# Optimization experiments

Hardware: AMD Instinct MI355X
Metric: run time of the kernel (lower is better)

## Reference

```python
import jax, jax.numpy as jnp
import numpy as np
from itertools import product as _prod

B = 2          # batch size
NPB = 4096     # voxels per batch
C = 384        # input_dim
H = 8          # num_heads
OUT = 32       # output_dim (seg classes)
SPATIAL = (32, 256, 256)
POOL_R = np.array([1, 2, 2, 2])    # [1]+query_gs_ratio
COMP_R = np.array([1, 16, 16, 16])  # [1]+compress_ratio


def _coords():
    rng = np.random.default_rng(0)
    rows = []
    for b in range(B):
        cand = np.stack([rng.integers(0, s, 4 * NPB) for s in SPATIAL], 1)
        cand = np.unique(cand, axis=0)
        sel = cand[rng.permutation(len(cand))[:NPB]]
        rows.append(np.concatenate([np.full((NPB, 1), b, np.int64), sel], 1))
    return np.concatenate(rows).astype(np.int32)


def setup_inputs() -> dict:
    idx = _coords()                     # [N,4] unique (b,z,y,x)
    N = idx.shape[0]
    pool_u, pool_inv = np.unique(idx // POOL_R, axis=0, return_inverse=True)
    emb_u, emb_inv = np.unique(idx // COMP_R, axis=0, return_inverse=True)
    # submanifold 3x3x3 neighbor table (same batch), -1 = missing
    lut = {tuple(r): i for i, r in enumerate(idx.tolist())}
    nbr = np.full((N, 27), -1, np.int32)
    rows = idx.tolist()
    for k, (dz, dy, dx) in enumerate(_prod((-1, 0, 1), repeat=3)):
        for i, (b, z, y, x) in enumerate(rows):
            nbr[i, k] = lut.get((b, z + dz, y + dy, x + dx), -1)
    key = jax.random.key(0)
    ks = jax.random.split(key, 12)
    g = lambda k, shp, s: jax.random.normal(k, shp, jnp.float32) * s
    s = 1.0 / float(np.sqrt(C))
    return dict(
        feats=g(ks[0], (N, C), 1.0),
        W_pool=g(ks[1], (C, C), s), b_pool=jnp.zeros((C,), jnp.float32),
        W_emb=g(ks[2], (C, C), s), b_emb=jnp.zeros((C,), jnp.float32),
        Wq=g(ks[3], (C, C), s), bq=jnp.zeros((C,), jnp.float32),
        Wk=g(ks[4], (C, C), s), bk=jnp.zeros((C,), jnp.float32),
        Wv=g(ks[5], (C, C), s), bv=jnp.zeros((C,), jnp.float32),
        Wo=g(ks[6], (C, C), s), bo=jnp.zeros((C,), jnp.float32),
        W_conv=g(ks[7], (27, C, OUT), 1.0 / float(np.sqrt(27 * C))),
        b_conv=jnp.zeros((OUT,), jnp.float32),
        pool_inv=jnp.asarray(pool_inv, jnp.int32),
        pool_coords=jnp.asarray(pool_u, jnp.int32),
        emb_inv=jnp.asarray(emb_inv, jnp.int32),
        emb_coords=jnp.asarray(emb_u, jnp.int32),
        nbr_idx=jnp.asarray(nbr),
        batch_size=B,
    )


def _sine_pe(xyz, d_pos):
    # xyz: [n,3] normalized to [0,1]; PositionEmbeddingCoordsSine (3detr-style)
    cdim = d_pos // xyz.shape[1]
    dim_t = 10000.0 ** (2.0 * (jnp.arange(cdim) // 2).astype(jnp.float32) / cdim)
    emb = (xyz * (2.0 * jnp.pi))[:, :, None] / dim_t          # [n,3,cdim]
    pe = jnp.stack([jnp.sin(emb[..., 0::2]), jnp.cos(emb[..., 1::2])], -1)
    return pe.reshape(xyz.shape[0], -1)                        # [n,d_pos]


def reference(feats, W_pool, b_pool, W_emb, b_emb, Wq, bq, Wk, bk, Wv, bv,
              Wo, bo, W_conv, b_conv, pool_inv, pool_coords, emb_inv,
              emb_coords, nbr_idx, batch_size):
    Mp, Me, Cc = pool_coords.shape[0], emb_coords.shape[0], feats.shape[1]
    hd = Cc // H
    # query path: linear + scatter_max over pool cells
    pool_f = jax.ops.segment_max(feats @ W_pool + b_pool, pool_inv, num_segments=Mp)
    # kv path: linear + scatter_max over compressed cells (coords of argmax rows
    # within a cell all equal the unique cell coord, so mean == unique coord)
    emb_f = jax.ops.segment_max(feats @ W_emb + b_emb, emb_inv, num_segments=Me)
    # per-batch min/max-normalized sine positional encoding on concat(emb,pool)
    emb_xyz = emb_coords[:, 1:].astype(jnp.float32)
    pool_xyz = pool_coords[:, 1:].astype(jnp.float32)
    all_xyz = jnp.concatenate([emb_xyz, pool_xyz], 0)
    bids = jnp.concatenate([emb_coords[:, 0], pool_coords[:, 0]], 0)
    mins = jax.ops.segment_min(all_xyz, bids, num_segments=batch_size)
    maxs = jax.ops.segment_max(all_xyz, bids, num_segments=batch_size)
    norm = (all_xyz - mins[bids]) / (maxs[bids] - mins[bids] + 1e-6)
    pe = _sine_pe(norm, Cc)
    emb_f = emb_f + pe[:Me]
    pool_f = pool_f + pe[Me:]
    # multi-head cross-attention, masked to same-batch pairs
    q = (pool_f @ Wq + bq).reshape(Mp, H, hd)
    k = (emb_f @ Wk + bk).reshape(Me, H, hd)
    v = (emb_f @ Wv + bv).reshape(Me, H, hd)
    scores = jnp.einsum('phd,ehd->hpe', q, k) / jnp.sqrt(jnp.float32(hd))
    same_b = pool_coords[:, 0][None, :, None] == emb_coords[:, 0][None, None, :]
    attn = jax.nn.softmax(jnp.where(same_b, scores, -1e9), axis=-1)
    o = jnp.einsum('hpe,ehd->phd', attn, v).reshape(Mp, Cc) @ Wo + bo
    # broadcast back to voxels + residual
    new_f = feats + o[pool_inv]
    # SubMConv3d seg head: gather 27 neighbors, contract with kernel
    valid = (nbr_idx >= 0)[:, :, None]
    gathered = jnp.where(valid, new_f[jnp.maximum(nbr_idx, 0)], 0.0)  # [N,27,C]
    logits = jnp.einsum('nkc,kco->no', gathered, W_conv) + b_conv
    return logits
```

## Files before the change

kernel.cpp:

```cpp
#include <hip/hip_runtime.h>
#include <hip/hip_bf16.h>
#include <math.h>

#define CDIM 384
#define NHEAD 8
#define HD 48
#define OUTD 32
#define MAXB 16
#define CONVK 10368

typedef __bf16 bf16x8 __attribute__((ext_vector_type(8)));
typedef float f32x4 __attribute__((ext_vector_type(4)));

__device__ __forceinline__ f32x4 mfma16(bf16x8 a, bf16x8 b, f32x4 c) {
  return __builtin_amdgcn_mfma_f32_16x16x32_bf16(a, b, c, 0, 0, 0);
}
__device__ __forceinline__ bf16x8 zero8() {
  bf16x8 z = {(__bf16)0.f, (__bf16)0.f, (__bf16)0.f, (__bf16)0.f,
              (__bf16)0.f, (__bf16)0.f, (__bf16)0.f, (__bf16)0.f};
  return z;
}

__device__ __forceinline__ unsigned enc_f(float f) {
  unsigned u = __float_as_uint(f);
  return (u & 0x80000000u) ? ~u : (u | 0x80000000u);
}
__device__ __forceinline__ float dec_f(unsigned u) {
  unsigned v = (u & 0x80000000u) ? (u ^ 0x80000000u) : ~u;
  return __uint_as_float(v);
}

__global__ __launch_bounds__(256) void prep_kernel(
    const float* __restrict__ feats, __hip_bfloat16* __restrict__ feats16, int N,
    const float* __restrict__ W_pool, const float* __restrict__ W_emb,
    const float* __restrict__ Wk, const float* __restrict__ Wv,
    const float* __restrict__ Wq, const float* __restrict__ Wo,
    __hip_bfloat16* __restrict__ Wt_pe, __hip_bfloat16* __restrict__ Wt_kv,
    __hip_bfloat16* __restrict__ Wt_q, __hip_bfloat16* __restrict__ Wt_o,
    const float* __restrict__ Wc, __hip_bfloat16* __restrict__ Wct,
    __hip_bfloat16* __restrict__ vt, int Mepad,
    const int* __restrict__ ec, const int* __restrict__ pc, int Mp, int Me,
    const int* __restrict__ bsz, int* smin, int* smax, int* ebv,
    int nbF, int nbW, int nbC, int nbV, int nbM) {
  __shared__ int lmin[MAXB * 3], lmax[MAXB * 3];
  int b = blockIdx.x;
  int t = threadIdx.x;
  if (b < nbF) {
    int v = b * 256 + t;
    if (v < N * 48) {
      float4 a0 = *reinterpret_cast<const float4*>(feats + (size_t)v * 8);
      float4 a1 = *reinterpret_cast<const float4*>(feats + (size_t)v * 8 + 4);
      __hip_bfloat16 tmp[8] = {
        __float2bfloat16(a0.x), __float2bfloat16(a0.y), __float2bfloat16(a0.z), __float2bfloat16(a0.w),
        __float2bfloat16(a1.x), __float2bfloat16(a1.y), __float2bfloat16(a1.z), __float2bfloat16(a1.w)};
      *reinterpret_cast<bf16x8*>(feats16 + (size_t)v * 8) = *reinterpret_cast<const bf16x8*>(tmp);
    }
    return;
  }
  b -= nbF;
  if (b < 6 * nbW) {
    int m = b / nbW;
    int v = (b - m * nbW) * 256 + t;
    if (v >= CDIM * 48) return;
    const float* src;
    __hip_bfloat16* dst;
    switch (m) {
      case 0: src = W_pool; dst = Wt_pe; break;
      case 1: src = W_emb;  dst = Wt_pe + (size_t)CDIM * CDIM; break;
      case 2: src = Wk;     dst = Wt_kv; break;
      case 3: src = Wv;     dst = Wt_kv + (size_t)CDIM * CDIM; break;
      case 4: src = Wq;     dst = Wt_q; break;
      default: src = Wo;    dst = Wt_o; break;
    }
    int k8i = v / CDIM;
    int n = v - k8i * CDIM;
    int k8 = k8i * 8;
    __hip_bfloat16 tmp[8];
    #pragma unroll
    for (int u = 0; u < 8; ++u) tmp[u] = __float2bfloat16(src[(size_t)(k8 + u) * CDIM + n]);
    *reinterpret_cast<bf16x8*>(dst + (size_t)n * CDIM + k8) = *reinterpret_cast<const bf16x8*>(tmp);
    return;
  }
  b -= 6 * nbW;
  if (b < nbC) {
    int v = b * 256 + t;
    if (v >= OUTD * (CONVK / 8)) return;
    int k8i = v >> 5;
    int n = v & 31;
    int k8 = k8i * 8;
    __hip_bfloat16 tmp[8];
    #pragma unroll
    for (int u = 0; u < 8; ++u) tmp[u] = __float2bfloat16(Wc[(size_t)(k8 + u) * OUTD + n]);
    *reinterpret_cast<bf16x8*>(Wct + (size_t)n * CONVK + k8) = *reinterpret_cast<const bf16x8*>(tmp);
    return;
  }
  b -= nbC;
  if (b < nbV) {
    int v = b * 256 + t;
    if (v < NHEAD * Mepad) {
      int h = v / Mepad, e = v - h * Mepad;
      vt[(size_t)(h * 64 + HD) * Mepad + e] = __float2bfloat16(1.0f);
    }
    return;
  }
  b -= nbV;
  if (b < nbM) {
    if (t < MAXB * 3) { lmin[t] = 0x7fffffff; lmax[t] = (int)0x80000000; }
    __syncthreads();
    int i = b * 256 + t;
    int tot = Me + Mp;
    if (i < tot) {
      const int* r = (i < Me) ? (ec + 4 * i) : (pc + 4 * (i - Me));
      int bb = r[0];
      #pragma unroll
      for (int d = 0; d < 3; ++d) {
        atomicMin(&lmin[bb * 3 + d], r[1 + d]);
        atomicMax(&lmax[bb * 3 + d], r[1 + d]);
      }
    }
    __syncthreads();
    if (t < MAXB * 3) {
      if (lmin[t] != 0x7fffffff) atomicMin(&smin[t], lmin[t]);
      if (lmax[t] != (int)0x80000000) atomicMax(&smax[t], lmax[t]);
    }
    return;
  }
  b -= nbM;
  {
    int e = b * 256 + t;
    if (e == 0) { ebv[0] = 0; ebv[bsz[0]] = Me; }
    if (e > 0 && e < Me) {
      int b0 = ec[4 * (e - 1)], b1 = ec[4 * e];
      for (int bb = b0 + 1; bb <= b1; ++bb) ebv[bb] = e;
    }
  }
}

__global__ void pe_kernel(const unsigned* __restrict__ encP, const unsigned* __restrict__ encE,
                          __hip_bfloat16* __restrict__ pool16, __hip_bfloat16* __restrict__ emb16,
                          const int* __restrict__ pc, int Mp,
                          const int* __restrict__ ec, int Me,
                          const int* __restrict__ smin, const int* __restrict__ smax) {
  int gid = blockIdx.x * blockDim.x + threadIdx.x;
  int total = (Mp + Me) * CDIM;
  if (gid >= total) return;
  int row = gid / CDIM, c = gid - row * CDIM;
  const int* coords;
  const unsigned* src;
  __hip_bfloat16* dst;
  int lrow;
  if (row < Me) { lrow = row; coords = ec + 4 * row; src = encE; dst = emb16; }
  else { lrow = row - Me; coords = pc + 4 * lrow; src = encP; dst = pool16; }
  int b = coords[0];
  int dim = c >> 7;
  int i = c & 127;
  int j = i >> 1;
  float x = (float)coords[1 + dim];
  float mn = (float)smin[b * 3 + dim];
  float mx = (float)smax[b * 3 + dim];
  float nrm = (x - mn) / (mx - mn + 1e-6f);
  float freq = exp2f(-(float)j * 0.20762050593046014f);
  float arg = nrm * 6.283185307179586f * freq;
  float pe = (i & 1) ? cosf(arg) : sinf(arg);
  float val = dec_f(src[(size_t)lrow * CDIM + c]) + pe;
  dst[(size_t)lrow * CDIM + c] = __float2bfloat16(val);
}

template <int EPI>
__global__ __launch_bounds__(256) void mgemm_kernel(
    const __hip_bfloat16* __restrict__ A, int M,
    const __hip_bfloat16* __restrict__ Wt,
    const float* __restrict__ bias0, const float* __restrict__ bias1,
    void* __restrict__ d0, void* __restrict__ d1,
    const int* __restrict__ inv0, const int* __restrict__ inv1,
    int Mepad) {
  __shared__ __align__(16) __hip_bfloat16 As[128][72];
  __shared__ __align__(16) __hip_bfloat16 Bs[64][72];
  const int m0 = blockIdx.x * 128;
  const int n0 = blockIdx.y * 64;
  const int t = threadIdx.x;
  const int lane = t & 63, w = t >> 6;
  const int wr = w >> 1, wc = w & 1;
  const int lq = lane & 15, lg = lane >> 4;

  f32x4 acc[4][2];
  #pragma unroll
  for (int i = 0; i < 4; ++i) {
    acc[i][0] = (f32x4){0.f, 0.f, 0.f, 0.f};
    acc[i][1] = (f32x4){0.f, 0.f, 0.f, 0.f};
  }
  const int arow = t >> 3;
  const int acol = (t & 7) * 8;

  for (int k0 = 0; k0 < CDIM; k0 += 64) {
    #pragma unroll
    for (int i = 0; i < 4; ++i) {
      int r = arow + i * 32;
      int gr = m0 + r;
      bf16x8 val = zero8();
      if (gr < M) val = *reinterpret_cast<const bf16x8*>(A + (size_t)gr * CDIM + k0 + acol);
      *reinterpret_cast<bf16x8*>(&As[r][acol]) = val;
    }
    #pragma unroll
    for (int i = 0; i < 2; ++i) {
      int r = arow + i * 32;
      bf16x8 val = *reinterpret_cast<const bf16x8*>(Wt + (size_t)(n0 + r) * CDIM + k0 + acol);
      *reinterpret_cast<bf16x8*>(&Bs[r][acol]) = val;
    }
    __syncthreads();
    #pragma unroll
    for (int ks = 0; ks < 2; ++ks) {
      bf16x8 af[4], bfv[2];
      #pragma unroll
      for (int fm = 0; fm < 4; ++fm)
        af[fm] = *reinterpret_cast<const bf16x8*>(&As[wr * 64 + fm * 16 + lq][ks * 32 + lg * 8]);
      #pragma unroll
      for (int fn = 0; fn < 2; ++fn)
        bfv[fn] = *reinterpret_cast<const bf16x8*>(&Bs[wc * 32 + fn * 16 + lq][ks * 32 + lg * 8]);
      #pragma unroll
      for (int fm = 0; fm < 4; ++fm)
        #pragma unroll
        for (int fn = 0; fn < 2; ++fn)
          acc[fm][fn] = mfma16(af[fm], bfv[fn], acc[fm][fn]);
    }
    __syncthreads();
  }

  const bool sec = (n0 >= CDIM);
  const int nb = n0 - (sec ? CDIM : 0) + wc * 32;
  const int nA = nb + lq, nB = nb + 16 + lq;

  if (EPI == 0) {
    const float* bias = sec ? bias1 : bias0;
    unsigned* dst = (unsigned*)(sec ? d1 : d0);
    const int* inv = sec ? inv1 : inv0;
    float bA = bias[nA], bB = bias[nB];
    #pragma unroll
    for (int fm = 0; fm < 4; ++fm) {
      int rbase = m0 + wr * 64 + fm * 16 + lg * 4;
      int cs = -1;
      float mA = 0.f, mB = 0.f;
      #pragma unroll
      for (int j = 0; j < 4; ++j) {
        int r = rbase + j;
        if (r < M) {
          int s = inv[r];
          float vA = acc[fm][0][j] + bA;
          float vB = acc[fm][1][j] + bB;
          if (s == cs) { mA = fmaxf(mA, vA); mB = fmaxf(mB, vB); }
          else {
            if (cs >= 0) {
              atomicMax(&dst[(size_t)cs * CDIM + nA], enc_f(mA));
              atomicMax(&dst[(size_t)cs * CDIM + nB], enc_f(mB));
            }
            cs = s; mA = vA; mB = vB;
          }
        }
      }
      if (cs >= 0) {
        atomicMax(&dst[(size_t)cs * CDIM + nA], enc_f(mA));
        atomicMax(&dst[(size_t)cs * CDIM + nB], enc_f(mB));
      }
    }
  } else if (EPI == 1) {
    float bA = bias0[nA], bB = bias0[nB];
    float* dst = (float*)d0;
    #pragma unroll
    for (int fm = 0; fm < 4; ++fm)
      #pragma unroll
      for (int j = 0; j < 4; ++j) {
        int r = m0 + wr * 64 + fm * 16 + lg * 4 + j;
        if (r < M) {
          dst[(size_t)r * CDIM + nA] = acc[fm][0][j] + bA;
          dst[(size_t)r * CDIM + nB] = acc[fm][1][j] + bB;
        }
      }
  } else if (EPI == 2) {
    const float scale = 0.2082350914f;
    float bA = bias0[nA], bB = bias0[nB];
    int hA = nA / HD, dA = nA - hA * HD;
    int hB = nB / HD, dB = nB - hB * HD;
    __hip_bfloat16* dst = (__hip_bfloat16*)d0;
    #pragma unroll
    for (int fm = 0; fm < 4; ++fm)
      #pragma unroll
      for (int j = 0; j < 4; ++j) {
        int r = m0 + wr * 64 + fm * 16 + lg * 4 + j;
        if (r < M) {
          dst[(size_t)r * 512 + hA * 64 + dA] = __float2bfloat16((acc[fm][0][j] + bA) * scale);
          dst[(size_t)r * 512 + hB * 64 + dB] = __float2bfloat16((acc[fm][1][j] + bB) * scale);
        }
      }
  } else {
    if (!sec) {
      float bA = bias0[nA], bB = bias0[nB];
      int hA = nA / HD, dA = nA - hA * HD;
      int hB = nB / HD, dB = nB - hB * HD;
      __hip_bfloat16* dst = (__hip_bfloat16*)d0;
      #pragma unroll
      for (int fm = 0; fm < 4; ++fm)
        #pragma unroll
        for (int j = 0; j < 4; ++j) {
          int r = m0 + wr * 64 + fm * 16 + lg * 4 + j;
          if (r < M) {
            dst[(size_t)r * 512 + hA * 64 + dA] = __float2bfloat16(acc[fm][0][j] + bA);
            dst[(size_t)r * 512 + hB * 64 + dB] = __float2bfloat16(acc[fm][1][j] + bB);
          }
        }
    } else {
      float bA = bias1[nA], bB = bias1[nB];
      int hA = nA / HD, dA = nA - hA * HD;
      int hB = nB / HD, dB = nB - hB * HD;
      __hip_bfloat16* dst = (__hip_bfloat16*)d1;
      #pragma unroll
      for (int fm = 0; fm < 4; ++fm)
        #pragma unroll
        for (int j = 0; j < 4; ++j) {
          int r = m0 + wr * 64 + fm * 16 + lg * 4 + j;
          if (r < M) {
            dst[(size_t)(hA * 64 + dA) * Mepad + r] = __float2bfloat16(acc[fm][0][j] + bA);
            dst[(size_t)(hB * 64 + dB) * Mepad + r] = __float2bfloat16(acc[fm][1][j] + bB);
          }
        }
    }
  }
}

__global__ __launch_bounds__(256) void attn_mfma_kernel(
    const __hip_bfloat16* __restrict__ qb, const __hip_bfloat16* __restrict__ kb,
    const __hip_bfloat16* __restrict__ vt, int Mepad,
    const int* __restrict__ pc, const int* __restrict__ eb,
    int Mp, int Me, __hip_bfloat16* __restrict__ ob) {
  __shared__ __align__(16) __hip_bfloat16 Ks[64][72];
  __shared__ __align__(16) __hip_bfloat16 Vs[64][72];
  __shared__ __align__(16) __hip_bfloat16 pl[4][16][72];
  __shared__ int sred[4][4];
  const int h = blockIdx.y;
  const int t = threadIdx.x;
  const int wv = t >> 6, lane = t & 63;
  const int lq = lane & 15, lg = lane >> 4;
  const int q0 = blockIdx.x * 64 + wv * 16;

  int lo[4], hi[4];
  #pragma unroll
  for (int r = 0; r < 4; ++r) {
    int q = q0 + lg * 4 + r;
    if (q < Mp) { int b = pc[4 * q]; lo[r] = eb[b]; hi[r] = eb[b + 1]; }
    else { lo[r] = 0x7fffffff; hi[r] = 0; }
  }
  int lomin = min(min(lo[0], lo[1]), min(lo[2], lo[3]));
  int lomax = max(max(lo[0], lo[1]), max(lo[2], lo[3]));
  int himin = min(min(hi[0], hi[1]), min(hi[2], hi[3]));
  int himax = max(max(hi[0], hi[1]), max(hi[2], hi[3]));
  #pragma unroll
  for (int off = 1; off < 64; off <<= 1) {
    lomin = min(lomin, __shfl_xor(lomin, off));
    lomax = max(lomax, __shfl_xor(lomax, off));
    himin = min(himin, __shfl_xor(himin, off));
    himax = max(himax, __shfl_xor(himax, off));
  }
  if (lane == 0) {
    sred[wv][0] = lomin; sred[wv][1] = lomax;
    sred[wv][2] = himin; sred[wv][3] = himax;
  }
  __syncthreads();
  lomin = min(min(sred[0][0], sred[1][0]), min(sred[2][0], sred[3][0]));
  lomax = max(max(sred[0][1], sred[1][1]), max(sred[2][1], sred[3][1]));
  himin = min(min(sred[0][2], sred[1][2]), min(sred[2][2], sred[3][2]));
  himax = max(max(sred[0][3], sred[1][3]), max(sred[2][3], sred[3][3]));

  int qrow = min(q0 + lq, Mp - 1);
  const __hip_bfloat16* qp = qb + (size_t)qrow * 512 + h * 64 + lg * 8;
  bf16x8 aq0 = *reinterpret_cast<const bf16x8*>(qp);
  bf16x8 aq1 = *reinterpret_cast<const bf16x8*>(qp + 32);

  const int str = t >> 2;
  const int stc = (t & 3) * 16;
  const __hip_bfloat16* vrow = vt + (size_t)(h * 64 + str) * Mepad + stc;

  f32x4 zero = {0.f, 0.f, 0.f, 0.f};
  f32x4 oacc[4];
  oacc[0] = zero; oacc[1] = zero; oacc[2] = zero; oacc[3] = zero;

  bf16x8 k0, k1, v0, v1;
  auto load_tile = [&](int e0) {
    int er = e0 + str;
    k0 = zero8(); k1 = zero8();
    if (er < Me) {
      const __hip_bfloat16* kp = kb + (size_t)er * 512 + h * 64 + stc;
      k0 = *reinterpret_cast<const bf16x8*>(kp);
      k1 = *reinterpret_cast<const bf16x8*>(kp + 8);
    }
    v0 = *reinterpret_cast<const bf16x8*>(vrow + e0);
    v1 = *reinterpret_cast<const bf16x8*>(vrow + e0 + 8);
  };
  const int e0beg = lomin & ~63;
  load_tile(e0beg);

  for (int e0 = e0beg; e0 < himax; e0 += 64) {
    __syncthreads();
    *reinterpret_cast<bf16x8*>(&Ks[str][stc]) = k0;
    *reinterpret_cast<bf16x8*>(&Ks[str][stc + 8]) = k1;
    *reinterpret_cast<bf16x8*>(&Vs[str][stc]) = v0;
    *reinterpret_cast<bf16x8*>(&Vs[str][stc + 8]) = v1;
    __syncthreads();
    if (e0 + 64 < himax) load_tile(e0 + 64);

    f32x4 sf[4];
    #pragma unroll
    for (int s = 0; s < 4; ++s) {
      bf16x8 bk0 = *reinterpret_cast<const bf16x8*>(&Ks[s * 16 + lq][lg * 8]);
      bf16x8 bk1 = *reinterpret_cast<const bf16x8*>(&Ks[s * 16 + lq][32 + lg * 8]);
      f32x4 z = zero;
      z = mfma16(aq0, bk0, z);
      z = mfma16(aq1, bk1, z);
      sf[s] = z;
    }
    const bool interior = (e0 >= lomax) && (e0 + 64 <= himin);
    if (interior) {
      #pragma unroll
      for (int s = 0; s < 4; ++s)
        #pragma unroll
        for (int r = 0; r < 4; ++r)
          pl[wv][lg * 4 + r][s * 16 + lq] = __float2bfloat16(exp2f(sf[s][r]));
    } else {
      #pragma unroll
      for (int s = 0; s < 4; ++s) {
        int e = e0 + s * 16 + lq;
        #pragma unroll
        for (int r = 0; r < 4; ++r) {
          bool m = (e >= lo[r]) && (e < hi[r]);
          float p = m ? exp2f(sf[s][r]) : 0.f;
          pl[wv][lg * 4 + r][s * 16 + lq] = __float2bfloat16(p);
        }
      }
    }
    asm volatile("s_waitcnt lgkmcnt(0)" ::: "memory");
    __builtin_amdgcn_sched_barrier(0);
    #pragma unroll
    for (int ks = 0; ks < 2; ++ks) {
      bf16x8 ap = *reinterpret_cast<const bf16x8*>(&pl[wv][lq][ks * 32 + lg * 8]);
      #pragma unroll
      for (int dt = 0; dt < 4; ++dt) {
        bf16x8 bv = *reinterpret_cast<const bf16x8*>(&Vs[dt * 16 + lq][ks * 32 + lg * 8]);
        oacc[dt] = mfma16(ap, bv, oacc[dt]);
      }
    }
  }

  #pragma unroll
  for (int r = 0; r < 4; ++r) {
    float l = __shfl(oacc[3][r], (lane & 48));
    int q = q0 + lg * 4 + r;
    if (q < Mp && l > 0.f) {
      float inv = 1.0f / l;
      __hip_bfloat16* op = ob + (size_t)q * CDIM + h * HD;
      op[lq]      = __float2bfloat16(oacc[0][r] * inv);
      op[16 + lq] = __float2bfloat16(oacc[1][r] * inv);
      op[32 + lq] = __float2bfloat16(oacc[2][r] * inv);
    }
  }
}

__global__ void newf16_kernel(const float* __restrict__ feats, const float* __restrict__ o2,
                              const int* __restrict__ pinv, __hip_bfloat16* __restrict__ nf,
                              int N) {
  int v = blockIdx.x * 256 + threadIdx.x;
  if (v >= N * 48) return;
  int n = v / 48, c8 = (v - n * 48) * 8;
  const float* fp = feats + (size_t)n * CDIM + c8;
  const float* op = o2 + (size_t)pinv[n] * CDIM + c8;
  float4 a0 = *reinterpret_cast<const float4*>(fp);
  float4 a1 = *reinterpret_cast<const float4*>(fp + 4);
  float4 b0 = *reinterpret_cast<const float4*>(op);
  float4 b1 = *reinterpret_cast<const float4*>(op + 4);
  __hip_bfloat16 tmp[8] = {
    __float2bfloat16(a0.x + b0.x), __float2bfloat16(a0.y + b0.y),
    __float2bfloat16(a0.z + b0.z), __float2bfloat16(a0.w + b0.w),
    __float2bfloat16(a1.x + b1.x), __float2bfloat16(a1.y + b1.y),
    __float2bfloat16(a1.z + b1.z), __float2bfloat16(a1.w + b1.w)};
  *reinterpret_cast<bf16x8*>(nf + (size_t)v * 8) = *reinterpret_cast<const bf16x8*>(tmp);
}

__global__ __launch_bounds__(256) void mconv_kernel(
    const __hip_bfloat16* __restrict__ nf, const int* __restrict__ nbr,
    const __hip_bfloat16* __restrict__ Wct, float* __restrict__ outp, int N) {
  __shared__ __align__(16) __hip_bfloat16 As[128][72];
  __shared__ __align__(16) __hip_bfloat16 Bs[32][72];
  __shared__ int jrow[128];
  const int n0 = blockIdx.x * 128;
  const int kg = blockIdx.y;
  const int t = threadIdx.x;
  const int lane = t & 63, w = t >> 6;
  const int lq = lane & 15, lg = lane >> 4;
  f32x4 acc[2][2];
  acc[0][0] = (f32x4){0.f,0.f,0.f,0.f}; acc[0][1] = acc[0][0];
  acc[1][0] = acc[0][0]; acc[1][1] = acc[0][0];
  const int arow = t >> 3, acol = (t & 7) * 8;

  for (int kk = kg * 3; kk < kg * 3 + 3; ++kk) {
    __syncthreads();
    if (t < 128) {
      int n = n0 + t;
      jrow[t] = (n < N) ? nbr[(size_t)n * 27 + kk] : -1;
    }
    __syncthreads();
    for (int c0 = 0; c0 < CDIM; c0 += 64) {
      #pragma unroll
      for (int i = 0; i < 4; ++i) {
        int r = arow + i * 32;
        int j = jrow[r];
        bf16x8 val = zero8();
        if (j >= 0) val = *reinterpret_cast<const bf16x8*>(nf + (size_t)j * CDIM + c0 + acol);
        *reinterpret_cast<bf16x8*>(&As[r][acol]) = val;
      }
      {
        int r = t >> 3;
        bf16x8 val = *reinterpret_cast<const bf16x8*>(Wct + (size_t)r * CONVK + kk * CDIM + c0 + acol);
        *reinterpret_cast<bf16x8*>(&Bs[r][acol]) = val;
      }
      __syncthreads();
      #pragma unroll
      for (int ks = 0; ks < 2; ++ks) {
        bf16x8 af[2], bfv[2];
        #pragma unroll
        for (int fm = 0; fm < 2; ++fm)
          af[fm] = *reinterpret_cast<const bf16x8*>(&As[w * 32 + fm * 16 + lq][ks * 32 + lg * 8]);
        #pragma unroll
        for (int fn = 0; fn < 2; ++fn)
          bfv[fn] = *reinterpret_cast<const bf16x8*>(&Bs[fn * 16 + lq][ks * 32 + lg * 8]);
        #pragma unroll
        for (int fm = 0; fm < 2; ++fm)
          #pragma unroll
          for (int fn = 0; fn < 2; ++fn)
            acc[fm][fn] = mfma16(af[fm], bfv[fn], acc[fm][fn]);
      }
      __syncthreads();
    }
  }
  #pragma unroll
  for (int fm = 0; fm < 2; ++fm)
    #pragma unroll
    for (int j = 0; j < 4; ++j) {
      int r = n0 + w * 32 + fm * 16 + lg * 4 + j;
      if (r < N) {
        #pragma unroll
        for (int fn = 0; fn < 2; ++fn)
          outp[((size_t)kg * N + r) * OUTD + fn * 16 + lq] = acc[fm][fn][j];
      }
    }
}

__global__ void conv_reduce_kernel(const float* __restrict__ outp,
                                   const float* __restrict__ bc,
                                   float* __restrict__ out, int N) {
  int v = blockIdx.x * 256 + threadIdx.x;
  if (v >= N * OUTD) return;
  int oo = v & (OUTD - 1);
  float s = bc[oo];
  #pragma unroll
  for (int kg = 0; kg < 9; ++kg) s += outp[(size_t)kg * N * OUTD + v];
  out[v] = s;
}

extern "C" void kernel_launch(void* const* d_in, const int* in_sizes, int n_in,
                              void* d_out, int out_size, void* d_ws, size_t ws_size,
                              hipStream_t stream) {
  const float* feats  = (const float*)d_in[0];
  const float* W_pool = (const float*)d_in[1];
  const float* b_pool = (const float*)d_in[2];
  const float* W_emb  = (const float*)d_in[3];
  const float* b_emb  = (const float*)d_in[4];
  const float* Wq = (const float*)d_in[5];  const float* bq = (const float*)d_in[6];
  const float* Wk = (const float*)d_in[7];  const float* bk = (const float*)d_in[8];
  const float* Wv = (const float*)d_in[9];  const float* bv = (const float*)d_in[10];
  const float* Wo = (const float*)d_in[11]; const float* bo = (const float*)d_in[12];
  const float* Wc = (const float*)d_in[13]; const float* bc = (const float*)d_in[14];
  const int* pool_inv    = (const int*)d_in[15];
  const int* pool_coords = (const int*)d_in[16];
  const int* emb_inv     = (const int*)d_in[17];
  const int* emb_coords  = (const int*)d_in[18];
  const int* nbr         = (const int*)d_in[19];
  const int* bsz         = (const int*)d_in[20];
  int N  = in_sizes[0] / CDIM;
  int Mp = in_sizes[16] / 4;
  int Me = in_sizes[18] / 4;
  int Mepad = ((Me >> 6) + 2) << 6;

  char* wsb = (char*)d_ws;
  size_t off = 0;
  auto alloc = [&](size_t bytes) { void* p = wsb + off; off += (bytes + 255) & ~(size_t)255; return p; };
  unsigned* encA = (unsigned*)alloc((size_t)Mp * CDIM * 4);
  unsigned* encB = (unsigned*)alloc((size_t)Me * CDIM * 4);
  __hip_bfloat16* vt = (__hip_bfloat16*)alloc((size_t)512 * Mepad * 2);
  size_t zspan1 = off;
  __hip_bfloat16* pool16  = (__hip_bfloat16*)alloc((size_t)Mp * CDIM * 2);
  __hip_bfloat16* emb16   = (__hip_bfloat16*)alloc((size_t)Me * CDIM * 2);
  __hip_bfloat16* feats16 = (__hip_bfloat16*)alloc((size_t)N * CDIM * 2);
  float* o2 = (float*)alloc((size_t)Mp * CDIM * 4 > (size_t)9 * N * OUTD * 4
                                ? (size_t)Mp * CDIM * 4 : (size_t)9 * N * OUTD * 4);
  __hip_bfloat16* Wt_pe = (__hip_bfloat16*)alloc((size_t)768 * CDIM * 2);
  __hip_bfloat16* Wt_kv = (__hip_bfloat16*)alloc((size_t)768 * CDIM * 2);
  __hip_bfloat16* Wt_q  = (__hip_bfloat16*)alloc((size_t)CDIM * CDIM * 2);
  __hip_bfloat16* Wt_o  = (__hip_bfloat16*)alloc((size_t)CDIM * CDIM * 2);
  __hip_bfloat16* Wct   = (__hip_bfloat16*)alloc((size_t)OUTD * CONVK * 2);
  int* smin = (int*)alloc(MAXB * 3 * 4);
  int* smax = (int*)alloc(MAXB * 3 * 4);
  int* eb   = (int*)alloc((MAXB + 1) * 4);

  __hip_bfloat16* q16  = (__hip_bfloat16*)encA;
  __hip_bfloat16* k16  = (__hip_bfloat16*)encB;
  __hip_bfloat16* ob16 = pool16;
  __hip_bfloat16* newf16 = feats16;
  float* outp = o2;

  hipMemsetAsync(wsb, 0, zspan1, stream);
  hipMemsetAsync(smin, 0x7f, MAXB * 3 * 4, stream);
  hipMemsetAsync(smax, 0x80, MAXB * 3 * 4, stream);

  int nbF = (N * 48 + 255) / 256;
  int nbW = (CDIM * 48 + 255) / 256;
  int nbC = (OUTD * (CONVK / 8) + 255) / 256;
  int nbV = (NHEAD * Mepad + 255) / 256;
  int nbM = (Mp + Me + 255) / 256;
  int nbE = (Me + 255) / 256;
  prep_kernel<<<nbF + 6 * nbW + nbC + nbV + nbM + nbE, 256, 0, stream>>>(
      feats, feats16, N, W_pool, W_emb, Wk, Wv, Wq, Wo,
      Wt_pe, Wt_kv, Wt_q, Wt_o, Wc, Wct, vt, Mepad,
      emb_coords, pool_coords, Mp, Me, bsz, smin, smax, eb,
      nbF, nbW, nbC, nbV, nbM);

  mgemm_kernel<0><<<dim3((N + 127) / 128, 12), 256, 0, stream>>>(
      feats16, N, Wt_pe, b_pool, b_emb, encA, encB, pool_inv, emb_inv, 0);
  pe_kernel<<<((Mp + Me) * CDIM + 255) / 256, 256, 0, stream>>>(
      encA, encB, pool16, emb16, pool_coords, Mp, emb_coords, Me, smin, smax);

  hipMemsetAsync(encA, 0, (size_t)((char*)encB - (char*)encA) + (size_t)Me * 1024, stream);

  mgemm_kernel<2><<<dim3((Mp + 127) / 128, 6), 256, 0, stream>>>(
      pool16, Mp, Wt_q, bq, nullptr, q16, nullptr, nullptr, nullptr, 0);
  mgemm_kernel<3><<<dim3((Me + 127) / 128, 12), 256, 0, stream>>>(
      emb16, Me, Wt_kv, bk, bv, k16, vt, nullptr, nullptr, Mepad);

  attn_mfma_kernel<<<dim3((Mp + 63) / 64, NHEAD), 256, 0, stream>>>(
      q16, k16, vt, Mepad, pool_coords, eb, Mp, Me, ob16);

  mgemm_kernel<1><<<dim3((Mp + 127) / 128, 6), 256, 0, stream>>>(
      ob16, Mp, Wt_o, bo, nullptr, o2, nullptr, nullptr, nullptr, 0);

  newf16_kernel<<<(N * 48 + 255) / 256, 256, 0, stream>>>(feats, o2, pool_inv, newf16, N);

  mconv_kernel<<<dim3((N + 127) / 128, 9), 256, 0, stream>>>(newf16, nbr, Wct, outp, N);
  conv_reduce_kernel<<<(N * OUTD + 255) / 256, 256, 0, stream>>>(outp, bc, (float*)d_out, N);
}
```

Before: 192.5 us.

## Merge Q and KV projections into one launch, double-buffer attention tiles

The Q and KV projection GEMMs now run in a single launch that splits work by flat block index. The memset of the padded head columns is dropped, and the blocks with n0==0 zero those padding lanes instead. The attention kernel double-buffers its K/V shared-memory tiles, which removes one __syncthreads per iteration and lets the global load run two tiles ahead. The positional encoding also switches to fast __sinf/__cosf intrinsics, trading some accuracy for fewer instructions. Together these aim to cut launch and memset overhead and barrier stalls in attention, at the cost of more shared memory per block and a less precise encoding.

After: 163.6 us. 15.0% less time.

```diff
diff --git a/kernel.cpp b/kernel.cpp
--- a/kernel.cpp
+++ b/kernel.cpp
@@ -161,23 +161,23 @@
   float nrm = (x - mn) / (mx - mn + 1e-6f);
   float freq = exp2f(-(float)j * 0.20762050593046014f);
   float arg = nrm * 6.283185307179586f * freq;
-  float pe = (i & 1) ? cosf(arg) : sinf(arg);
+  float pe = (i & 1) ? __cosf(arg) : __sinf(arg);
   float val = dec_f(src[(size_t)lrow * CDIM + c]) + pe;
   dst[(size_t)lrow * CDIM + c] = __float2bfloat16(val);
 }
 
 template <int EPI>
-__global__ __launch_bounds__(256) void mgemm_kernel(
+__device__ __forceinline__ void mgemm_body(
+    int bx, int by,
+    __hip_bfloat16 (*As)[72], __hip_bfloat16 (*Bs)[72],
     const __hip_bfloat16* __restrict__ A, int M,
     const __hip_bfloat16* __restrict__ Wt,
     const float* __restrict__ bias0, const float* __restrict__ bias1,
     void* __restrict__ d0, void* __restrict__ d1,
     const int* __restrict__ inv0, const int* __restrict__ inv1,
     int Mepad) {
-  __shared__ __align__(16) __hip_bfloat16 As[128][72];
-  __shared__ __align__(16) __hip_bfloat16 Bs[64][72];
-  const int m0 = blockIdx.x * 128;
-  const int n0 = blockIdx.y * 64;
+  const int m0 = bx * 128;
+  const int n0 = by * 64;
   const int t = threadIdx.x;
   const int lane = t & 63, w = t >> 6;
   const int wr = w >> 1, wc = w & 1;
@@ -324,6 +324,56 @@
         }
     }
   }
+  if ((EPI == 2 || EPI == 3) && n0 == 0) {
+    __hip_bfloat16* dst = (__hip_bfloat16*)d0;
+    for (int c = t; c < 1024; c += 256) {
+      int r = m0 + (c >> 3);
+      int hh = c & 7;
+      if (r < M) {
+        bf16x8 z = zero8();
+        *reinterpret_cast<bf16x8*>(dst + (size_t)r * 512 + hh * 64 + 48) = z;
+        *reinterpret_cast<bf16x8*>(dst + (size_t)r * 512 + hh * 64 + 56) = z;
+      }
+    }
+  }
+}
+
+__global__ __launch_bounds__(256) void mgemm0_kernel(
+    const __hip_bfloat16* __restrict__ A, int M, const __hip_bfloat16* __restrict__ Wt,
+    const float* __restrict__ bias0, const float* __restrict__ bias1,
+    unsigned* __restrict__ d0, unsigned* __restrict__ d1,
+    const int* __restrict__ inv0, const int* __restrict__ inv1) {
+  __shared__ __align__(16) __hip_bfloat16 As[128][72];
+  __shared__ __align__(16) __hip_bfloat16 Bs[64][72];
+  mgemm_body<0>(blockIdx.x, blockIdx.y, As, Bs, A, M, Wt, bias0, bias1, d0, d1, inv0, inv1, 0);
+}
+
+__global__ __launch_bounds__(256) void mgemm1_kernel(
+    const __hip_bfloat16* __restrict__ A, int M, const __hip_bfloat16* __restrict__ Wt,
+    const float* __restrict__ bias0, float* __restrict__ d0) {
+  __shared__ __align__(16) __hip_bfloat16 As[128][72];
+  __shared__ __align__(16) __hip_bfloat16 Bs[64][72];
+  mgemm_body<1>(blockIdx.x, blockIdx.y, As, Bs, A, M, Wt, bias0, nullptr, d0, nullptr, nullptr, nullptr, 0);
+}
+
+__global__ __launch_bounds__(256) void qkv_kernel(
+    const __hip_bfloat16* __restrict__ pool16, int Mp, const __hip_bfloat16* __restrict__ Wt_q,
+    const float* __restrict__ bq,
+    const __hip_bfloat16* __restrict__ emb16, int Me, const __hip_bfloat16* __restrict__ Wt_kv,
+    const float* __restrict__ bk, const float* __restrict__ bv,
+    __hip_bfloat16* __restrict__ q16, __hip_bfloat16* __restrict__ k16,
+    __hip_bfloat16* __restrict__ vt, int Mepad, int nbQ, int gxQ, int gxK) {
+  __shared__ __align__(16) __hip_bfloat16 As[128][72];
+  __shared__ __align__(16) __hip_bfloat16 Bs[64][72];
+  int b = blockIdx.x;
+  if (b < nbQ) {
+    mgemm_body<2>(b % gxQ, b / gxQ, As, Bs, pool16, Mp, Wt_q, bq, nullptr,
+                  q16, nullptr, nullptr, nullptr, 0);
+  } else {
+    b -= nbQ;
+    mgemm_body<3>(b % gxK, b / gxK, As, Bs, emb16, Me, Wt_kv, bk, bv,
+                  k16, vt, nullptr, nullptr, Mepad);
+  }
 }
 
 __global__ __launch_bounds__(256) void attn_mfma_kernel(
@@ -331,8 +381,8 @@
     const __hip_bfloat16* __restrict__ vt, int Mepad,
     const int* __restrict__ pc, const int* __restrict__ eb,
     int Mp, int Me, __hip_bfloat16* __restrict__ ob) {
-  __shared__ __align__(16) __hip_bfloat16 Ks[64][72];
-  __shared__ __align__(16) __hip_bfloat16 Vs[64][72];
+  __shared__ __align__(16) __hip_bfloat16 Ks[2][64][72];
+  __shared__ __align__(16) __hip_bfloat16 Vs[2][64][72];
   __shared__ __align__(16) __hip_bfloat16 pl[4][16][72];
   __shared__ int sred[4][4];
   const int h = blockIdx.y;
@@ -394,23 +444,31 @@
     v0 = *reinterpret_cast<const bf16x8*>(vrow + e0);
     v1 = *reinterpret_cast<const bf16x8*>(vrow + e0 + 8);
   };
+  auto store_tile = [&](int nb) {
+    *reinterpret_cast<bf16x8*>(&Ks[nb][str][stc]) = k0;
+    *reinterpret_cast<bf16x8*>(&Ks[nb][str][stc + 8]) = k1;
+    *reinterpret_cast<bf16x8*>(&Vs[nb][str][stc]) = v0;
+    *reinterpret_cast<bf16x8*>(&Vs[nb][str][stc + 8]) = v1;
+  };
   const int e0beg = lomin & ~63;
   load_tile(e0beg);
-
-  for (int e0 = e0beg; e0 < himax; e0 += 64) {
+  store_tile(0);
+  if (e0beg + 64 < himax) load_tile(e0beg + 64);
+
+  int it = 0;
+  for (int e0 = e0beg; e0 < himax; e0 += 64, ++it) {
     __syncthreads();
-    *reinterpret_cast<bf16x8*>(&Ks[str][stc]) = k0;
-    *reinterpret_cast<bf16x8*>(&Ks[str][stc + 8]) = k1;
-    *reinterpret_cast<bf16x8*>(&Vs[str][stc]) = v0;
-    *reinterpret_cast<bf16x8*>(&Vs[str][stc + 8]) = v1;
-    __syncthreads();
-    if (e0 + 64 < himax) load_tile(e0 + 64);
+    const int cur = it & 1;
+    if (e0 + 64 < himax) {
+      store_tile(cur ^ 1);
+      if (e0 + 128 < himax) load_tile(e0 + 128);
+    }
 
     f32x4 sf[4];
     #pragma unroll
     for (int s = 0; s < 4; ++s) {
-      bf16x8 bk0 = *reinterpret_cast<const bf16x8*>(&Ks[s * 16 + lq][lg * 8]);
-      bf16x8 bk1 = *reinterpret_cast<const bf16x8*>(&Ks[s * 16 + lq][32 + lg * 8]);
+      bf16x8 bk0 = *reinterpret_cast<const bf16x8*>(&Ks[cur][s * 16 + lq][lg * 8]);
+      bf16x8 bk1 = *reinterpret_cast<const bf16x8*>(&Ks[cur][s * 16 + lq][32 + lg * 8]);
       f32x4 z = zero;
       z = mfma16(aq0, bk0, z);
       z = mfma16(aq1, bk1, z);
@@ -442,7 +500,7 @@
       bf16x8 ap = *reinterpret_cast<const bf16x8*>(&pl[wv][lq][ks * 32 + lg * 8]);
       #pragma unroll
       for (int dt = 0; dt < 4; ++dt) {
-        bf16x8 bv = *reinterpret_cast<const bf16x8*>(&Vs[dt * 16 + lq][ks * 32 + lg * 8]);
+        bf16x8 bv = *reinterpret_cast<const bf16x8*>(&Vs[cur][dt * 16 + lq][ks * 32 + lg * 8]);
         oacc[dt] = mfma16(ap, bv, oacc[dt]);
       }
     }
@@ -630,23 +688,24 @@
       emb_coords, pool_coords, Mp, Me, bsz, smin, smax, eb,
       nbF, nbW, nbC, nbV, nbM);
 
-  mgemm_kernel<0><<<dim3((N + 127) / 128, 12), 256, 0, stream>>>(
-      feats16, N, Wt_pe, b_pool, b_emb, encA, encB, pool_inv, emb_inv, 0);
+  mgemm0_kernel<<<dim3((N + 127) / 128, 12), 256, 0, stream>>>(
+      feats16, N, Wt_pe, b_pool, b_emb, encA, encB, pool_inv, emb_inv);
   pe_kernel<<<((Mp + Me) * CDIM + 255) / 256, 256, 0, stream>>>(
       encA, encB, pool16, emb16, pool_coords, Mp, emb_coords, Me, smin, smax);
 
-  hipMemsetAsync(encA, 0, (size_t)((char*)encB - (char*)encA) + (size_t)Me * 1024, stream);
-
-  mgemm_kernel<2><<<dim3((Mp + 127) / 128, 6), 256, 0, stream>>>(
-      pool16, Mp, Wt_q, bq, nullptr, q16, nullptr, nullptr, nullptr, 0);
-  mgemm_kernel<3><<<dim3((Me + 127) / 128, 12), 256, 0, stream>>>(
-      emb16, Me, Wt_kv, bk, bv, k16, vt, nullptr, nullptr, Mepad);
+  {
+    int gxQ = (Mp + 127) / 128, gxK = (Me + 127) / 128;
+    int nbQ = gxQ * 6;
+    qkv_kernel<<<nbQ + gxK * 12, 256, 0, stream>>>(
+        pool16, Mp, Wt_q, bq, emb16, Me, Wt_kv, bk, bv,
+        q16, k16, vt, Mepad, nbQ, gxQ, gxK);
+  }
 
   attn_mfma_kernel<<<dim3((Mp + 63) / 64, NHEAD), 256, 0, stream>>>(
       q16, k16, vt, Mepad, pool_coords, eb, Mp, Me, ob16);
 
-  mgemm_kernel<1><<<dim3((Mp + 127) / 128, 6), 256, 0, stream>>>(
-      ob16, Mp, Wt_o, bo, nullptr, o2, nullptr, nullptr, nullptr, 0);
+  mgemm1_kernel<<<dim3((Mp + 127) / 128, 6), 256, 0, stream>>>(
+      ob16, Mp, Wt_o, bo, o2);
 
   newf16_kernel<<<(N * 48 + 255) / 256, 256, 0, stream>>>(feats, o2, pool_inv, newf16, N);
 
```
